# Performance work log

Measured on AMD Instinct MI355X. Metric: run time of the kernel, lower is better.

The kernel has to match this reference:

```python
import jax, jax.numpy as jnp
import numpy as np
import math

D_MODEL = 1024
NUM_HEADS = 16
D_HEAD = D_MODEL // NUM_HEADS  # 64
B, S = 2, 1024


def setup_inputs() -> dict:
    key = jax.random.key(0)
    ks = jax.random.split(key, 11)
    s = 1.0 / math.sqrt(D_MODEL)
    inp = {
        "Q": jax.random.normal(ks[0], (B, S, D_MODEL), jnp.float32),
        "K": jax.random.normal(ks[1], (B, S, D_MODEL), jnp.float32),
        "V": jax.random.normal(ks[2], (B, S, D_MODEL), jnp.float32),
        "Wq": jax.random.normal(ks[3], (D_MODEL, D_MODEL), jnp.float32) * s,
        "bq": jnp.zeros((D_MODEL,), jnp.float32),
        "Wk": jax.random.normal(ks[4], (D_MODEL, D_MODEL), jnp.float32) * s,
        "bk": jnp.zeros((D_MODEL,), jnp.float32),
        "Wv": jax.random.normal(ks[5], (D_MODEL, D_MODEL), jnp.float32) * s,
        "bv": jnp.zeros((D_MODEL,), jnp.float32),
        "Wo": jax.random.normal(ks[6], (D_MODEL, D_MODEL), jnp.float32) * s,
        "bo": jnp.zeros((D_MODEL,), jnp.float32),
    }
    return inp


def _linear(x, W, b):
    # torch nn.Linear: x @ W.T + b
    return jnp.einsum("bsd,ed->bse", x, W) + b


def _split_heads(x):
    # Faithful to original: view(b, s, d_head, num_heads).transpose(1, 2)
    # -> 'heads' axis has size d_head, per-head dim is num_heads.
    b, s, _ = x.shape
    return x.reshape(b, s, D_HEAD, NUM_HEADS).transpose(0, 2, 1, 3)  # [b, d_head, s, num_heads]


def reference(Q, K, V, Wq, bq, Wk, bk, Wv, bv, Wo, bo):
    q = _split_heads(_linear(Q, Wq, bq))  # [b, h=d_head, s, e=num_heads]
    k = _split_heads(_linear(K, Wk, bk))
    v = _split_heads(_linear(V, Wv, bv))
    scale = 1.0 / math.sqrt(D_MODEL)  # original scales by sqrt(d_model)
    scores = jnp.einsum("bhqe,bhke->bhqk", q, k) * scale
    attn = jax.nn.softmax(scores, axis=-1)
    ctx = jnp.einsum("bhqk,bhke->bhqe", attn, v)  # [b, d_head, s, num_heads]
    # combine_heads: transpose(1,2) then flatten last two dims
    b, h, s, e = ctx.shape
    merged = ctx.transpose(0, 2, 1, 3).reshape(b, s, h * e)
    return _linear(merged, Wo, bo)
```

## Files before the change

### kernel.cpp

```cpp
#include <hip/hip_runtime.h>
#include <cstdint>
#include <cstddef>
#include <math.h>

typedef _Float16 f16;
typedef _Float16 f16x8 __attribute__((ext_vector_type(8)));
typedef _Float16 f16x4 __attribute__((ext_vector_type(4)));
typedef float f32x4 __attribute__((ext_vector_type(4)));
typedef float f32x16 __attribute__((ext_vector_type(16)));

#define MFMA16(A, B, C) __builtin_amdgcn_mfma_f32_16x16x32_f16((A), (B), (C), 0, 0, 0)
#define MFMA32(A, B, C) __builtin_amdgcn_mfma_f32_32x32x16_f16((A), (B), (C), 0, 0, 0)

#if __has_builtin(__builtin_amdgcn_exp2f)
#define EXP2(x) __builtin_amdgcn_exp2f(x)
#else
#define EXP2(x) exp2f(x)
#endif

__device__ __forceinline__ f16x8 ld8(const f16* p) { return *(const f16x8*)p; }
__device__ __forceinline__ void st8(f16* p, f16x8 v) { *(f16x8*)p = v; }
__device__ __forceinline__ void st4(f16* p, f16x4 v) { *(f16x4*)p = v; }

__device__ __forceinline__ void gll16(const f16* g, f16* l) {
    __builtin_amdgcn_global_load_lds(
        (__attribute__((address_space(1))) void*)(uintptr_t)g,
        (__attribute__((address_space(3))) void*)(unsigned)(uintptr_t)l,
        16, 0, 0);
}

__global__ __launch_bounds__(256) void cast_all(
    const float* __restrict__ Q, const float* __restrict__ K, const float* __restrict__ V,
    const float* __restrict__ Wq, const float* __restrict__ Wk, const float* __restrict__ Wv,
    const float* __restrict__ Wo, f16* __restrict__ dst)
{
    size_t e = ((size_t)blockIdx.x * 256 + threadIdx.x) * 8;
    const float* s; size_t r;
    if (e < 2097152)      { s = Q;  r = e; }
    else if (e < 4194304) { s = K;  r = e - 2097152; }
    else if (e < 6291456) { s = V;  r = e - 4194304; }
    else if (e < 7340032) { s = Wq; r = e - 6291456; }
    else if (e < 8388608) { s = Wk; r = e - 7340032; }
    else if (e < 9437184) { s = Wv; r = e - 8388608; }
    else                  { s = Wo; r = e - 9437184; }
    float4 a = *(const float4*)(s + r);
    float4 b = *(const float4*)(s + r + 4);
    f16x8 o;
    o[0]=(f16)a.x; o[1]=(f16)a.y; o[2]=(f16)a.z; o[3]=(f16)a.w;
    o[4]=(f16)b.x; o[5]=(f16)b.y; o[6]=(f16)b.z; o[7]=(f16)b.w;
    st8(dst + e, o);
}

__global__ __launch_bounds__(256) void qkv_gemm(
    const f16* __restrict__ ws, const float* __restrict__ bq,
    const float* __restrict__ bk, const float* __restrict__ bv,
    f16* __restrict__ outbase)
{
    const int bx = blockIdx.x, bm = blockIdx.y;
    const int mat = bx >> 3, bn = bx & 7;
    const f16* A  = ws + (size_t)mat * 2097152;
    const f16* Bw = ws + 6291456 + (size_t)mat * 1048576;
    const float* bias = (mat == 0) ? bq : (mat == 1) ? bk : bv;
    f16* C = outbase + (size_t)mat * 2097152;

    __shared__ f16 As[2 * 4096];
    __shared__ f16 Bs[2 * 8192];
    const int t = threadIdx.x;
    const int w = t >> 6, lane = t & 63, lg = lane >> 4, ll = lane & 15;
    const int swz = ((lane & 7) ^ (lane >> 3)) * 8;

    const f16* Ap = A  + (size_t)(bm * 64  + w * 8 + (lane >> 3)) * 1024 + swz;
    const f16* Bp = Bw + (size_t)(bn * 128 + w * 8 + (lane >> 3)) * 1024 + swz;

    f32x4 acc[4][2] = {};
    const int ll7 = ll & 7;

    {
        gll16(Ap,         &As[w * 512]);
        gll16(Ap + 32768, &As[2048 + w * 512]);
        #pragma unroll
        for (int q = 0; q < 4; ++q)
            gll16(Bp + q * 32768, &Bs[q * 2048 + w * 512]);
    }

    #pragma unroll 2
    for (int kt = 0; kt < 16; ++kt) {
        const int cur = kt & 1;
        __syncthreads();
        if (kt < 15) {
            const f16* Ak = Ap + (kt + 1) * 64;
            const f16* Bk = Bp + (kt + 1) * 64;
            f16* Ad = &As[(cur ^ 1) * 4096 + w * 512];
            f16* Bd = &Bs[(cur ^ 1) * 8192 + w * 512];
            gll16(Ak,         Ad);
            gll16(Ak + 32768, Ad + 2048);
            #pragma unroll
            for (int q = 0; q < 4; ++q)
                gll16(Bk + q * 32768, Bd + q * 2048);
        }
        const f16* Ac = &As[cur * 4096];
        const f16* Bc = &Bs[cur * 8192];
        #pragma unroll
        for (int ks = 0; ks < 2; ++ks) {
            f16x8 af[4], bf[2];
            #pragma unroll
            for (int i = 0; i < 4; ++i)
                af[i] = ld8(&Ac[(i * 16 + ll) * 64 + (((ks * 4 + lg) ^ ll7) * 8)]);
            #pragma unroll
            for (int j = 0; j < 2; ++j)
                bf[j] = ld8(&Bc[(w * 32 + j * 16 + ll) * 64 + (((ks * 4 + lg) ^ ll7) * 8)]);
            #pragma unroll
            for (int i = 0; i < 4; ++i)
                #pragma unroll
                for (int j = 0; j < 2; ++j)
                    acc[i][j] = MFMA16(af[i], bf[j], acc[i][j]);
        }
    }

    const float qscale = 0.04508422002778009f;
    #pragma unroll
    for (int j = 0; j < 2; ++j) {
        const int n = bn * 128 + w * 32 + j * 16 + ll;
        const float bv_ = bias[n];
        if (mat == 0) {
            #pragma unroll
            for (int i = 0; i < 4; ++i) {
                const int m0 = bm * 64 + i * 16 + lg * 4;
                #pragma unroll
                for (int r = 0; r < 4; ++r)
                    C[(size_t)(m0 + r) * 1024 + n] = (f16)((acc[i][j][r] + bv_) * qscale);
            }
        } else if (mat == 1) {
            #pragma unroll
            for (int i = 0; i < 4; ++i) {
                const int m0 = bm * 64 + i * 16 + lg * 4;
                #pragma unroll
                for (int r = 0; r < 4; ++r)
                    C[(size_t)(m0 + r) * 1024 + n] = (f16)(acc[i][j][r] + bv_);
            }
        } else {
            #pragma unroll
            for (int i = 0; i < 4; ++i) {
                const int m0 = bm * 64 + i * 16 + lg * 4;
                const int bb = m0 >> 10, s0 = m0 & 1023;
                f16x4 pv;
                pv[0] = (f16)(acc[i][j][0] + bv_);
                pv[1] = (f16)(acc[i][j][1] + bv_);
                pv[2] = (f16)(acc[i][j][2] + bv_);
                pv[3] = (f16)(acc[i][j][3] + bv_);
                st4(C + ((size_t)((bb * 64 + (n >> 4)) * 16 + (n & 15))) * 1024 + s0, pv);
            }
        }
    }
}

__global__ __launch_bounds__(256, 4) void attn(
    const f16* __restrict__ qlin, const f16* __restrict__ klin,
    const f16* __restrict__ vT, f16* __restrict__ merged)
{
    __shared__ f16 Ks[2][2048];
    __shared__ f16 Vs[2][2176];
    __shared__ f16 Ps[4][1280];

    const int t = threadIdx.x;
    const int w = t >> 6, lane = t & 63;
    const int l5 = lane & 31, hh = lane >> 5, lg = (lane >> 4) & 3, ll = lane & 15;
    const int h = blockIdx.x, qt = blockIdx.y, b = blockIdx.z;

    const int rowQ0 = b * 1024 + qt * 128;
    const int colh = h * 16;

    f16x8 qf = ld8(qlin + (size_t)(rowQ0 + w * 32 + l5) * 1024 + colh + hh * 8);

    const int sp = ((lane & 7) - (lane >> 3)) & 7;
    const f16* kptr = klin + (size_t)(b * 1024 + w * 32 + (lane >> 3) * 4 + (sp >> 1)) * 1024
                      + colh + (sp & 1) * 8;
    const int ve = t >> 4, vk = (t & 15) * 8;
    const f16* vptr = vT + (size_t)((b * 64 + h) * 16 + ve) * 1024 + vk;
    f16* vdst0 = &Vs[0][ve * 136 + vk];
    f16* vdst1 = &Vs[1][ve * 136 + vk];

    int offKa[4];
    #pragma unroll
    for (int mt = 0; mt < 4; ++mt) {
        const int r = mt * 32 + l5, g = r >> 2;
        offKa[mt] = g * 64 + (((((r & 3) * 2 + hh) + g) & 7) * 8);
    }

    float lsum = 0.f;
    f32x4 O0 = {}, O1 = {};
    f16* Pw = Ps[w];

    f16x8 vv = ld8(vptr);
    gll16(kptr, &Ks[0][w * 512]);
    st8(vdst0, vv);

    for (int kt = 0; kt < 8; ++kt) {
        const int cur = kt & 1;
        if (kt < 7) vv = ld8(vptr + (kt + 1) * 128);
        __syncthreads();
        if (kt < 7) {
            gll16(kptr + (size_t)(kt + 1) * 131072, &Ks[cur ^ 1][w * 512]);
            st8(cur ? vdst0 : vdst1, vv);
        }

        #pragma unroll
        for (int mt = 0; mt < 4; ++mt) {
            f16x8 ka = ld8(&Ks[cur][offKa[mt]]);
            f32x16 Sz = {};
            f32x16 S = MFMA32(ka, qf, Sz);

            #pragma unroll
            for (int g = 0; g < 4; ++g) {
                float p0 = EXP2(S[4 * g + 0]);
                float p1 = EXP2(S[4 * g + 1]);
                float p2 = EXP2(S[4 * g + 2]);
                float p3 = EXP2(S[4 * g + 3]);
                lsum += (p0 + p1) + (p2 + p3);
                f16x4 pk;
                pk[0] = (f16)p0; pk[1] = (f16)p1; pk[2] = (f16)p2; pk[3] = (f16)p3;
                st4(&Pw[l5 * 40 + g * 8 + hh * 4], pk);
            }

            f16x8 va  = ld8(&Vs[cur][ll * 136 + mt * 32 + lg * 8]);
            f16x8 pb0 = ld8(&Pw[ll * 40 + lg * 8]);
            f16x8 pb1 = ld8(&Pw[(16 + ll) * 40 + lg * 8]);
            O0 = MFMA16(va, pb0, O0);
            O1 = MFMA16(va, pb1, O1);
        }
    }

    lsum += __shfl_xor(lsum, 32);
    const float i0 = 1.f / __shfl(lsum, ll);
    const float i1 = 1.f / __shfl(lsum, 16 + ll);

    f16x4 o0, o1;
    o0[0]=(f16)(O0[0]*i0); o0[1]=(f16)(O0[1]*i0); o0[2]=(f16)(O0[2]*i0); o0[3]=(f16)(O0[3]*i0);
    o1[0]=(f16)(O1[0]*i1); o1[1]=(f16)(O1[1]*i1); o1[2]=(f16)(O1[2]*i1); o1[3]=(f16)(O1[3]*i1);
    const size_t q0 = rowQ0 + w * 32 + ll;
    st4(merged + q0 * 1024 + colh + lg * 4, o0);
    st4(merged + (q0 + 16) * 1024 + colh + lg * 4, o1);
}

__global__ __launch_bounds__(256) void o_gemm(
    const f16* __restrict__ A, const f16* __restrict__ Bw,
    const float* __restrict__ bias, float* __restrict__ Cf)
{
    const int bn = blockIdx.x, bm = blockIdx.y;
    __shared__ f16 As[2 * 4096];
    __shared__ f16 Bs[2 * 4096];
    const int t = threadIdx.x;
    const int w = t >> 6, lane = t & 63, lg = lane >> 4, ll = lane & 15;
    const int swz = ((lane & 7) ^ (lane >> 3)) * 8;

    const f16* Ap = A  + (size_t)(bm * 64 + w * 8 + (lane >> 3)) * 1024 + swz;
    const f16* Bp = Bw + (size_t)(bn * 64 + w * 8 + (lane >> 3)) * 1024 + swz;

    f32x4 acc[4] = {};
    const int ll7 = ll & 7;

    {
        gll16(Ap,         &As[w * 512]);
        gll16(Ap + 32768, &As[2048 + w * 512]);
        gll16(Bp,         &Bs[w * 512]);
        gll16(Bp + 32768, &Bs[2048 + w * 512]);
    }

    #pragma unroll 2
    for (int kt = 0; kt < 16; ++kt) {
        const int cur = kt & 1;
        __syncthreads();
        if (kt < 15) {
            const f16* Ak = Ap + (kt + 1) * 64;
            const f16* Bk = Bp + (kt + 1) * 64;
            f16* Ad = &As[(cur ^ 1) * 4096 + w * 512];
            f16* Bd = &Bs[(cur ^ 1) * 4096 + w * 512];
            gll16(Ak,         Ad);
            gll16(Ak + 32768, Ad + 2048);
            gll16(Bk,         Bd);
            gll16(Bk + 32768, Bd + 2048);
        }
        const f16* Ac = &As[cur * 4096];
        const f16* Bc = &Bs[cur * 4096];
        #pragma unroll
        for (int ks = 0; ks < 2; ++ks) {
            f16x8 af[4], bf;
            #pragma unroll
            for (int i = 0; i < 4; ++i)
                af[i] = ld8(&Ac[(i * 16 + ll) * 64 + (((ks * 4 + lg) ^ ll7) * 8)]);
            bf = ld8(&Bc[(w * 16 + ll) * 64 + (((ks * 4 + lg) ^ ll7) * 8)]);
            #pragma unroll
            for (int i = 0; i < 4; ++i)
                acc[i] = MFMA16(af[i], bf, acc[i]);
        }
    }

    const int n = bn * 64 + w * 16 + ll;
    const float bv_ = bias[n];
    #pragma unroll
    for (int i = 0; i < 4; ++i) {
        const int m0 = bm * 64 + i * 16 + lg * 4;
        #pragma unroll
        for (int r = 0; r < 4; ++r)
            Cf[(size_t)(m0 + r) * 1024 + n] = acc[i][r] + bv_;
    }
}

extern "C" void kernel_launch(void* const* d_in, const int* in_sizes, int n_in,
                              void* d_out, int out_size, void* d_ws, size_t ws_size,
                              hipStream_t stream) {
    (void)in_sizes; (void)n_in; (void)out_size; (void)ws_size;
    const float* Q  = (const float*)d_in[0];
    const float* K  = (const float*)d_in[1];
    const float* V  = (const float*)d_in[2];
    const float* Wq = (const float*)d_in[3];
    const float* bq = (const float*)d_in[4];
    const float* Wk = (const float*)d_in[5];
    const float* bk = (const float*)d_in[6];
    const float* Wv = (const float*)d_in[7];
    const float* bv = (const float*)d_in[8];
    const float* Wo = (const float*)d_in[9];
    const float* bo = (const float*)d_in[10];
    float* out = (float*)d_out;

    f16* ws = (f16*)d_ws;
    f16* qlin   = ws + 10485760;
    f16* klin   = ws + 12582912;
    f16* vT     = ws + 14680064;
    f16* merged = ws + 16777216;
    f16* Woc    = ws + 9437184;

    cast_all<<<5120, 256, 0, stream>>>(Q, K, V, Wq, Wk, Wv, Wo, ws);
    qkv_gemm<<<dim3(24, 32), 256, 0, stream>>>(ws, bq, bk, bv, qlin);
    attn<<<dim3(64, 8, 2), 256, 0, stream>>>(qlin, klin, vT, merged);
    o_gemm<<<dim3(16, 32), 256, 0, stream>>>(merged, Woc, bo, out);
}
```

Measured before the change: 159.8 us.

## Fuse fp32-to-fp16 casts into GEMM tile loads and drop cast kernel

```diff
diff --git a/kernel.cpp b/kernel.cpp
--- a/kernel.cpp
+++ b/kernel.cpp
@@ -29,128 +29,120 @@
         16, 0, 0);
 }
 
-__global__ __launch_bounds__(256) void cast_all(
-    const float* __restrict__ Q, const float* __restrict__ K, const float* __restrict__ V,
-    const float* __restrict__ Wq, const float* __restrict__ Wk, const float* __restrict__ Wv,
-    const float* __restrict__ Wo, f16* __restrict__ dst)
-{
-    size_t e = ((size_t)blockIdx.x * 256 + threadIdx.x) * 8;
-    const float* s; size_t r;
-    if (e < 2097152)      { s = Q;  r = e; }
-    else if (e < 4194304) { s = K;  r = e - 2097152; }
-    else if (e < 6291456) { s = V;  r = e - 4194304; }
-    else if (e < 7340032) { s = Wq; r = e - 6291456; }
-    else if (e < 8388608) { s = Wk; r = e - 7340032; }
-    else if (e < 9437184) { s = Wv; r = e - 8388608; }
-    else                  { s = Wo; r = e - 9437184; }
-    float4 a = *(const float4*)(s + r);
-    float4 b = *(const float4*)(s + r + 4);
+__device__ __forceinline__ f16x8 cvt8(float4 a, float4 b) {
     f16x8 o;
     o[0]=(f16)a.x; o[1]=(f16)a.y; o[2]=(f16)a.z; o[3]=(f16)a.w;
     o[4]=(f16)b.x; o[5]=(f16)b.y; o[6]=(f16)b.z; o[7]=(f16)b.w;
-    st8(dst + e, o);
-}
-
-__global__ __launch_bounds__(256) void qkv_gemm(
-    const f16* __restrict__ ws, const float* __restrict__ bq,
-    const float* __restrict__ bk, const float* __restrict__ bv,
+    return o;
+}
+
+#define QSCALE 0.04508422002778009f
+
+__global__ __launch_bounds__(256, 3) void qkv_gemm(
+    const float* __restrict__ Qf, const float* __restrict__ Kf, const float* __restrict__ Vf,
+    const float* __restrict__ Wq, const float* __restrict__ Wk, const float* __restrict__ Wv,
+    const float* __restrict__ bq, const float* __restrict__ bk, const float* __restrict__ bv,
     f16* __restrict__ outbase)
 {
     const int bx = blockIdx.x, bm = blockIdx.y;
     const int mat = bx >> 3, bn = bx & 7;
-    const f16* A  = ws + (size_t)mat * 2097152;
-    const f16* Bw = ws + 6291456 + (size_t)mat * 1048576;
+    const float* A = (mat == 0) ? Qf : (mat == 1) ? Kf : Vf;
+    const float* W = (mat == 0) ? Wq : (mat == 1) ? Wk : Wv;
     const float* bias = (mat == 0) ? bq : (mat == 1) ? bk : bv;
     f16* C = outbase + (size_t)mat * 2097152;
 
-    __shared__ f16 As[2 * 4096];
-    __shared__ f16 Bs[2 * 8192];
+    __shared__ f16 As[2][64 * 68];
+    __shared__ f16 Bs[2][128 * 68];
+
     const int t = threadIdx.x;
-    const int w = t >> 6, lane = t & 63, lg = lane >> 4, ll = lane & 15;
-    const int swz = ((lane & 7) ^ (lane >> 3)) * 8;
-
-    const f16* Ap = A  + (size_t)(bm * 64  + w * 8 + (lane >> 3)) * 1024 + swz;
-    const f16* Bp = Bw + (size_t)(bn * 128 + w * 8 + (lane >> 3)) * 1024 + swz;
-
-    f32x4 acc[4][2] = {};
-    const int ll7 = ll & 7;
-
-    {
-        gll16(Ap,         &As[w * 512]);
-        gll16(Ap + 32768, &As[2048 + w * 512]);
-        #pragma unroll
-        for (int q = 0; q < 4; ++q)
-            gll16(Bp + q * 32768, &Bs[q * 2048 + w * 512]);
-    }
-
-    #pragma unroll 2
+    const int w = t >> 6, lane = t & 63, l5 = lane & 31, hh = lane >> 5;
+
+    const int ra = t >> 2, qa = t & 3;
+    const int rb = t >> 1, hb = t & 1;
+    const float* Ag = A + (size_t)(bm * 64 + ra) * 1024 + qa * 16;
+    const float* Bg = W + (size_t)(bn * 128 + rb) * 1024 + hb * 32;
+    const int aoff = ra * 68 + qa * 16;
+    const int boff = rb * 68 + hb * 32;
+
+    f32x16 acc[2] = {};
+    float4 pa[4], pb[8];
+
+    #pragma unroll
+    for (int i = 0; i < 4; ++i) pa[i] = *(const float4*)(Ag + i * 4);
+    #pragma unroll
+    for (int i = 0; i < 8; ++i) pb[i] = *(const float4*)(Bg + i * 4);
+    st8(&As[0][aoff],     cvt8(pa[0], pa[1]));
+    st8(&As[0][aoff + 8], cvt8(pa[2], pa[3]));
+    st8(&Bs[0][boff],      cvt8(pb[0], pb[1]));
+    st8(&Bs[0][boff + 8],  cvt8(pb[2], pb[3]));
+    st8(&Bs[0][boff + 16], cvt8(pb[4], pb[5]));
+    st8(&Bs[0][boff + 24], cvt8(pb[6], pb[7]));
+    __syncthreads();
+
     for (int kt = 0; kt < 16; ++kt) {
         const int cur = kt & 1;
+        if (kt < 15) {
+            const float* Ak = Ag + (kt + 1) * 64;
+            const float* Bk = Bg + (kt + 1) * 64;
+            #pragma unroll
+            for (int i = 0; i < 4; ++i) pa[i] = *(const float4*)(Ak + i * 4);
+            #pragma unroll
+            for (int i = 0; i < 8; ++i) pb[i] = *(const float4*)(Bk + i * 4);
+        }
+        #pragma unroll
+        for (int ks = 0; ks < 4; ++ks) {
+            f16x8 bfr = ld8(&Bs[cur][(w * 32 + l5) * 68 + ks * 16 + hh * 8]);
+            f16x8 af0 = ld8(&As[cur][ l5        * 68 + ks * 16 + hh * 8]);
+            f16x8 af1 = ld8(&As[cur][(32 + l5)  * 68 + ks * 16 + hh * 8]);
+            acc[0] = MFMA32(af0, bfr, acc[0]);
+            acc[1] = MFMA32(af1, bfr, acc[1]);
+        }
+        if (kt < 15) {
+            f16* Ad = &As[cur ^ 1][aoff];
+            f16* Bd = &Bs[cur ^ 1][boff];
+            st8(Ad,     cvt8(pa[0], pa[1]));
+            st8(Ad + 8, cvt8(pa[2], pa[3]));
+            st8(Bd,      cvt8(pb[0], pb[1]));
+            st8(Bd + 8,  cvt8(pb[2], pb[3]));
+            st8(Bd + 16, cvt8(pb[4], pb[5]));
+            st8(Bd + 24, cvt8(pb[6], pb[7]));
+        }
         __syncthreads();
-        if (kt < 15) {
-            const f16* Ak = Ap + (kt + 1) * 64;
-            const f16* Bk = Bp + (kt + 1) * 64;
-            f16* Ad = &As[(cur ^ 1) * 4096 + w * 512];
-            f16* Bd = &Bs[(cur ^ 1) * 8192 + w * 512];
-            gll16(Ak,         Ad);
-            gll16(Ak + 32768, Ad + 2048);
-            #pragma unroll
-            for (int q = 0; q < 4; ++q)
-                gll16(Bk + q * 32768, Bd + q * 2048);
-        }
-        const f16* Ac = &As[cur * 4096];
-        const f16* Bc = &Bs[cur * 8192];
-        #pragma unroll
-        for (int ks = 0; ks < 2; ++ks) {
-            f16x8 af[4], bf[2];
-            #pragma unroll
-            for (int i = 0; i < 4; ++i)
-                af[i] = ld8(&Ac[(i * 16 + ll) * 64 + (((ks * 4 + lg) ^ ll7) * 8)]);
-            #pragma unroll
-            for (int j = 0; j < 2; ++j)
-                bf[j] = ld8(&Bc[(w * 32 + j * 16 + ll) * 64 + (((ks * 4 + lg) ^ ll7) * 8)]);
-            #pragma unroll
-            for (int i = 0; i < 4; ++i)
-                #pragma unroll
-                for (int j = 0; j < 2; ++j)
-                    acc[i][j] = MFMA16(af[i], bf[j], acc[i][j]);
-        }
-    }
-
-    const float qscale = 0.04508422002778009f;
-    #pragma unroll
-    for (int j = 0; j < 2; ++j) {
-        const int n = bn * 128 + w * 32 + j * 16 + ll;
-        const float bv_ = bias[n];
-        if (mat == 0) {
-            #pragma unroll
-            for (int i = 0; i < 4; ++i) {
-                const int m0 = bm * 64 + i * 16 + lg * 4;
-                #pragma unroll
-                for (int r = 0; r < 4; ++r)
-                    C[(size_t)(m0 + r) * 1024 + n] = (f16)((acc[i][j][r] + bv_) * qscale);
+    }
+
+    const int n = bn * 128 + w * 32 + l5;
+    const float bv_ = bias[n];
+    if (mat == 0) {
+        #pragma unroll
+        for (int i = 0; i < 2; ++i)
+            #pragma unroll
+            for (int r = 0; r < 16; ++r) {
+                const int m = bm * 64 + i * 32 + (r & 3) + 8 * (r >> 2) + 4 * hh;
+                C[(size_t)m * 1024 + n] = (f16)((acc[i][r] + bv_) * QSCALE);
             }
-        } else if (mat == 1) {
-            #pragma unroll
-            for (int i = 0; i < 4; ++i) {
-                const int m0 = bm * 64 + i * 16 + lg * 4;
-                #pragma unroll
-                for (int r = 0; r < 4; ++r)
-                    C[(size_t)(m0 + r) * 1024 + n] = (f16)(acc[i][j][r] + bv_);
+    } else if (mat == 1) {
+        #pragma unroll
+        for (int i = 0; i < 2; ++i)
+            #pragma unroll
+            for (int r = 0; r < 16; ++r) {
+                const int m = bm * 64 + i * 32 + (r & 3) + 8 * (r >> 2) + 4 * hh;
+                C[(size_t)m * 1024 + n] = (f16)(acc[i][r] + bv_);
             }
-        } else {
-            #pragma unroll
-            for (int i = 0; i < 4; ++i) {
-                const int m0 = bm * 64 + i * 16 + lg * 4;
+    } else {
+        const int hN = n >> 4, eN = n & 15;
+        #pragma unroll
+        for (int i = 0; i < 2; ++i)
+            #pragma unroll
+            for (int g = 0; g < 4; ++g) {
+                const int m0 = bm * 64 + i * 32 + 8 * g + 4 * hh;
                 const int bb = m0 >> 10, s0 = m0 & 1023;
                 f16x4 pv;
-                pv[0] = (f16)(acc[i][j][0] + bv_);
-                pv[1] = (f16)(acc[i][j][1] + bv_);
-                pv[2] = (f16)(acc[i][j][2] + bv_);
-                pv[3] = (f16)(acc[i][j][3] + bv_);
-                st4(C + ((size_t)((bb * 64 + (n >> 4)) * 16 + (n & 15))) * 1024 + s0, pv);
+                pv[0] = (f16)(acc[i][4 * g + 0] + bv_);
+                pv[1] = (f16)(acc[i][4 * g + 1] + bv_);
+                pv[2] = (f16)(acc[i][4 * g + 2] + bv_);
+                pv[3] = (f16)(acc[i][4 * g + 3] + bv_);
+                st4(C + ((size_t)((bb * 64 + hN) * 16 + eN)) * 1024 + s0, pv);
             }
-        }
     }
 }
 
@@ -243,66 +235,61 @@
 }
 
 __global__ __launch_bounds__(256) void o_gemm(
-    const f16* __restrict__ A, const f16* __restrict__ Bw,
-    const float* __restrict__ bias, float* __restrict__ Cf)
+    const f16* __restrict__ Am, const float* __restrict__ Wo,
+    const float* __restrict__ bo, float* __restrict__ Cf)
 {
     const int bn = blockIdx.x, bm = blockIdx.y;
-    __shared__ f16 As[2 * 4096];
-    __shared__ f16 Bs[2 * 4096];
+    __shared__ f16 As[2][64 * 68];
+    __shared__ f16 Bs[2][64 * 68];
     const int t = threadIdx.x;
-    const int w = t >> 6, lane = t & 63, lg = lane >> 4, ll = lane & 15;
-    const int swz = ((lane & 7) ^ (lane >> 3)) * 8;
-
-    const f16* Ap = A  + (size_t)(bm * 64 + w * 8 + (lane >> 3)) * 1024 + swz;
-    const f16* Bp = Bw + (size_t)(bn * 64 + w * 8 + (lane >> 3)) * 1024 + swz;
-
-    f32x4 acc[4] = {};
-    const int ll7 = ll & 7;
-
-    {
-        gll16(Ap,         &As[w * 512]);
-        gll16(Ap + 32768, &As[2048 + w * 512]);
-        gll16(Bp,         &Bs[w * 512]);
-        gll16(Bp + 32768, &Bs[2048 + w * 512]);
-    }
-
-    #pragma unroll 2
+    const int w = t >> 6, lane = t & 63, l5 = lane & 31, hh = lane >> 5;
+    const int wr = w >> 1, wc = w & 1;
+
+    const int ra = t >> 2, qa = t & 3;
+    const f16*   Ag = Am + (size_t)(bm * 64 + ra) * 1024 + qa * 16;
+    const float* Bg = Wo + (size_t)(bn * 64 + ra) * 1024 + qa * 16;
+    const int soff = ra * 68 + qa * 16;
+
+    f32x16 acc = {};
+    f16x8 la0, la1;
+    float4 pb[4];
+
+    la0 = ld8(Ag); la1 = ld8(Ag + 8);
+    #pragma unroll
+    for (int i = 0; i < 4; ++i) pb[i] = *(const float4*)(Bg + i * 4);
+    st8(&As[0][soff], la0); st8(&As[0][soff + 8], la1);
+    st8(&Bs[0][soff],     cvt8(pb[0], pb[1]));
+    st8(&Bs[0][soff + 8], cvt8(pb[2], pb[3]));
+    __syncthreads();
+
     for (int kt = 0; kt < 16; ++kt) {
         const int cur = kt & 1;
+        if (kt < 15) {
+            la0 = ld8(Ag + (kt + 1) * 64);
+            la1 = ld8(Ag + (kt + 1) * 64 + 8);
+            #pragma unroll
+            for (int i = 0; i < 4; ++i) pb[i] = *(const float4*)(Bg + (kt + 1) * 64 + i * 4);
+        }
+        #pragma unroll
+        for (int ks = 0; ks < 4; ++ks) {
+            f16x8 af = ld8(&As[cur][(wr * 32 + l5) * 68 + ks * 16 + hh * 8]);
+            f16x8 bf = ld8(&Bs[cur][(wc * 32 + l5) * 68 + ks * 16 + hh * 8]);
+            acc = MFMA32(af, bf, acc);
+        }
+        if (kt < 15) {
+            st8(&As[cur ^ 1][soff], la0); st8(&As[cur ^ 1][soff + 8], la1);
+            st8(&Bs[cur ^ 1][soff],     cvt8(pb[0], pb[1]));
+            st8(&Bs[cur ^ 1][soff + 8], cvt8(pb[2], pb[3]));
+        }
         __syncthreads();
-        if (kt < 15) {
-            const f16* Ak = Ap + (kt + 1) * 64;
-            const f16* Bk = Bp + (kt + 1) * 64;
-            f16* Ad = &As[(cur ^ 1) * 4096 + w * 512];
-            f16* Bd = &Bs[(cur ^ 1) * 4096 + w * 512];
-            gll16(Ak,         Ad);
-            gll16(Ak + 32768, Ad + 2048);
-            gll16(Bk,         Bd);
-            gll16(Bk + 32768, Bd + 2048);
-        }
-        const f16* Ac = &As[cur * 4096];
-        const f16* Bc = &Bs[cur * 4096];
-        #pragma unroll
-        for (int ks = 0; ks < 2; ++ks) {
-            f16x8 af[4], bf;
-            #pragma unroll
-            for (int i = 0; i < 4; ++i)
-                af[i] = ld8(&Ac[(i * 16 + ll) * 64 + (((ks * 4 + lg) ^ ll7) * 8)]);
-            bf = ld8(&Bc[(w * 16 + ll) * 64 + (((ks * 4 + lg) ^ ll7) * 8)]);
-            #pragma unroll
-            for (int i = 0; i < 4; ++i)
-                acc[i] = MFMA16(af[i], bf, acc[i]);
-        }
-    }
-
-    const int n = bn * 64 + w * 16 + ll;
-    const float bv_ = bias[n];
-    #pragma unroll
-    for (int i = 0; i < 4; ++i) {
-        const int m0 = bm * 64 + i * 16 + lg * 4;
-        #pragma unroll
-        for (int r = 0; r < 4; ++r)
-            Cf[(size_t)(m0 + r) * 1024 + n] = acc[i][r] + bv_;
+    }
+
+    const int n = bn * 64 + wc * 32 + l5;
+    const float bv_ = bo[n];
+    #pragma unroll
+    for (int r = 0; r < 16; ++r) {
+        const int m = bm * 64 + wr * 32 + (r & 3) + 8 * (r >> 2) + 4 * hh;
+        Cf[(size_t)m * 1024 + n] = acc[r] + bv_;
     }
 }
 
@@ -324,14 +311,12 @@
     float* out = (float*)d_out;
 
     f16* ws = (f16*)d_ws;
-    f16* qlin   = ws + 10485760;
-    f16* klin   = ws + 12582912;
-    f16* vT     = ws + 14680064;
-    f16* merged = ws + 16777216;
-    f16* Woc    = ws + 9437184;
-
-    cast_all<<<5120, 256, 0, stream>>>(Q, K, V, Wq, Wk, Wv, Wo, ws);
-    qkv_gemm<<<dim3(24, 32), 256, 0, stream>>>(ws, bq, bk, bv, qlin);
+    f16* qlin   = ws;
+    f16* klin   = ws + 2097152;
+    f16* vT     = ws + 4194304;
+    f16* merged = ws + 6291456;
+
+    qkv_gemm<<<dim3(24, 32), 256, 0, stream>>>(Q, K, V, Wq, Wk, Wv, bq, bk, bv, qlin);
     attn<<<dim3(64, 8, 2), 256, 0, stream>>>(qlin, klin, vT, merged);
-    o_gemm<<<dim3(16, 32), 256, 0, stream>>>(merged, Woc, bo, out);
-}
+    o_gemm<<<dim3(16, 32), 256, 0, stream>>>(merged, Wo, bo, out);
+}
```

Result: slower. 259.7 us (+62.5%).

## Fuse cast, QKV GEMM, attention and output GEMM into one persistent kernel

Applied to the files above, without the earlier changes.

```diff
diff --git a/kernel.cpp b/kernel.cpp
--- a/kernel.cpp
+++ b/kernel.cpp
@@ -17,6 +17,8 @@
 #else
 #define EXP2(x) exp2f(x)
 #endif
+
+#define NBLK 768
 
 __device__ __forceinline__ f16x8 ld8(const f16* p) { return *(const f16x8*)p; }
 __device__ __forceinline__ void st8(f16* p, f16x8 v) { *(f16x8*)p = v; }
@@ -29,280 +31,320 @@
         16, 0, 0);
 }
 
-__global__ __launch_bounds__(256) void cast_all(
+__device__ __forceinline__ void gridbarrier(int* flags, int phase) {
+    __syncthreads();
+    if (threadIdx.x == 0) {
+        __threadfence();
+        __hip_atomic_store(&flags[blockIdx.x], phase, __ATOMIC_RELEASE,
+                           __HIP_MEMORY_SCOPE_AGENT);
+    }
+    if (threadIdx.x < 64) {
+        for (;;) {
+            int ok = 1;
+            #pragma unroll
+            for (int i = 0; i < NBLK / 64; ++i) {
+                int v = __hip_atomic_load(&flags[threadIdx.x + i * 64],
+                                          __ATOMIC_RELAXED, __HIP_MEMORY_SCOPE_AGENT);
+                ok &= (v >= phase);
+            }
+            if (__all(ok)) break;
+            __builtin_amdgcn_s_sleep(4);
+        }
+    }
+    __syncthreads();
+    __threadfence();
+}
+
+#define QSCALE 0.04508422002778009f
+
+__global__ __launch_bounds__(256, 3) void fused(
     const float* __restrict__ Q, const float* __restrict__ K, const float* __restrict__ V,
-    const float* __restrict__ Wq, const float* __restrict__ Wk, const float* __restrict__ Wv,
-    const float* __restrict__ Wo, f16* __restrict__ dst)
+    const float* __restrict__ Wq, const float* __restrict__ bq,
+    const float* __restrict__ Wk, const float* __restrict__ bk,
+    const float* __restrict__ Wv, const float* __restrict__ bv,
+    const float* __restrict__ Wo, const float* __restrict__ bo,
+    f16* __restrict__ ws, float* __restrict__ out)
 {
-    size_t e = ((size_t)blockIdx.x * 256 + threadIdx.x) * 8;
-    const float* s; size_t r;
-    if (e < 2097152)      { s = Q;  r = e; }
-    else if (e < 4194304) { s = K;  r = e - 2097152; }
-    else if (e < 6291456) { s = V;  r = e - 4194304; }
-    else if (e < 7340032) { s = Wq; r = e - 6291456; }
-    else if (e < 8388608) { s = Wk; r = e - 7340032; }
-    else if (e < 9437184) { s = Wv; r = e - 8388608; }
-    else                  { s = Wo; r = e - 9437184; }
-    float4 a = *(const float4*)(s + r);
-    float4 b = *(const float4*)(s + r + 4);
-    f16x8 o;
-    o[0]=(f16)a.x; o[1]=(f16)a.y; o[2]=(f16)a.z; o[3]=(f16)a.w;
-    o[4]=(f16)b.x; o[5]=(f16)b.y; o[6]=(f16)b.z; o[7]=(f16)b.w;
-    st8(dst + e, o);
-}
-
-__global__ __launch_bounds__(256) void qkv_gemm(
-    const f16* __restrict__ ws, const float* __restrict__ bq,
-    const float* __restrict__ bk, const float* __restrict__ bv,
-    f16* __restrict__ outbase)
-{
-    const int bx = blockIdx.x, bm = blockIdx.y;
-    const int mat = bx >> 3, bn = bx & 7;
-    const f16* A  = ws + (size_t)mat * 2097152;
-    const f16* Bw = ws + 6291456 + (size_t)mat * 1048576;
-    const float* bias = (mat == 0) ? bq : (mat == 1) ? bk : bv;
-    f16* C = outbase + (size_t)mat * 2097152;
-
-    __shared__ f16 As[2 * 4096];
-    __shared__ f16 Bs[2 * 8192];
+    __shared__ union {
+        struct { f16 As[2 * 4096]; f16 Bs[2 * 8192]; } g;
+        struct { f16 Ks[2][2048]; f16 Vs[2][2176]; f16 Ps[4][1280]; } a;
+        struct { f16 As[2 * 4096]; f16 Bs[2 * 4096]; } o;
+    } sm;
+
+    int* flags = (int*)(ws + 18874368);
     const int t = threadIdx.x;
     const int w = t >> 6, lane = t & 63, lg = lane >> 4, ll = lane & 15;
-    const int swz = ((lane & 7) ^ (lane >> 3)) * 8;
-
-    const f16* Ap = A  + (size_t)(bm * 64  + w * 8 + (lane >> 3)) * 1024 + swz;
-    const f16* Bp = Bw + (size_t)(bn * 128 + w * 8 + (lane >> 3)) * 1024 + swz;
-
-    f32x4 acc[4][2] = {};
-    const int ll7 = ll & 7;
+
+    if (t == 0)
+        __hip_atomic_store(&flags[blockIdx.x], 0, __ATOMIC_RELAXED,
+                           __HIP_MEMORY_SCOPE_AGENT);
 
     {
+        f16* dst = ws;
+        #pragma unroll
+        for (int sweep = 0; sweep < 7; ++sweep) {
+            size_t e = ((size_t)sweep * NBLK * 256 + (size_t)blockIdx.x * 256 + t) * 8;
+            if (e < 10485760) {
+                const float* s; size_t r;
+                if (e < 2097152)      { s = Q;  r = e; }
+                else if (e < 4194304) { s = K;  r = e - 2097152; }
+                else if (e < 6291456) { s = V;  r = e - 4194304; }
+                else if (e < 7340032) { s = Wq; r = e - 6291456; }
+                else if (e < 8388608) { s = Wk; r = e - 7340032; }
+                else if (e < 9437184) { s = Wv; r = e - 8388608; }
+                else                  { s = Wo; r = e - 9437184; }
+                float4 a = *(const float4*)(s + r);
+                float4 b = *(const float4*)(s + r + 4);
+                f16x8 o;
+                o[0]=(f16)a.x; o[1]=(f16)a.y; o[2]=(f16)a.z; o[3]=(f16)a.w;
+                o[4]=(f16)b.x; o[5]=(f16)b.y; o[6]=(f16)b.z; o[7]=(f16)b.w;
+                st8(dst + e, o);
+            }
+        }
+    }
+    gridbarrier(flags, 1);
+
+    {
+        const int v = blockIdx.x;
+        const int bx = v % 24, bm = v / 24;
+        const int mat = bx >> 3, bn = bx & 7;
+        const f16* A  = ws + (size_t)mat * 2097152;
+        const f16* Bw = ws + 6291456 + (size_t)mat * 1048576;
+        const float* bias = (mat == 0) ? bq : (mat == 1) ? bk : bv;
+        f16* C = ws + 10485760 + (size_t)mat * 2097152;
+
+        f16* As = sm.g.As;
+        f16* Bs = sm.g.Bs;
+        const int swz = ((lane & 7) ^ (lane >> 3)) * 8;
+
+        const f16* Ap = A  + (size_t)(bm * 64  + w * 8 + (lane >> 3)) * 1024 + swz;
+        const f16* Bp = Bw + (size_t)(bn * 128 + w * 8 + (lane >> 3)) * 1024 + swz;
+
+        f32x4 acc[4][2] = {};
+        const int ll7 = ll & 7;
+
         gll16(Ap,         &As[w * 512]);
         gll16(Ap + 32768, &As[2048 + w * 512]);
         #pragma unroll
         for (int q = 0; q < 4; ++q)
             gll16(Bp + q * 32768, &Bs[q * 2048 + w * 512]);
-    }
-
-    #pragma unroll 2
-    for (int kt = 0; kt < 16; ++kt) {
-        const int cur = kt & 1;
-        __syncthreads();
-        if (kt < 15) {
-            const f16* Ak = Ap + (kt + 1) * 64;
-            const f16* Bk = Bp + (kt + 1) * 64;
-            f16* Ad = &As[(cur ^ 1) * 4096 + w * 512];
-            f16* Bd = &Bs[(cur ^ 1) * 8192 + w * 512];
-            gll16(Ak,         Ad);
-            gll16(Ak + 32768, Ad + 2048);
+
+        #pragma unroll 2
+        for (int kt = 0; kt < 16; ++kt) {
+            const int cur = kt & 1;
+            __syncthreads();
+            if (kt < 15) {
+                const f16* Ak = Ap + (kt + 1) * 64;
+                const f16* Bk = Bp + (kt + 1) * 64;
+                f16* Ad = &As[(cur ^ 1) * 4096 + w * 512];
+                f16* Bd = &Bs[(cur ^ 1) * 8192 + w * 512];
+                gll16(Ak,         Ad);
+                gll16(Ak + 32768, Ad + 2048);
+                #pragma unroll
+                for (int q = 0; q < 4; ++q)
+                    gll16(Bk + q * 32768, Bd + q * 2048);
+            }
+            const f16* Ac = &As[cur * 4096];
+            const f16* Bc = &Bs[cur * 8192];
             #pragma unroll
-            for (int q = 0; q < 4; ++q)
-                gll16(Bk + q * 32768, Bd + q * 2048);
-        }
-        const f16* Ac = &As[cur * 4096];
-        const f16* Bc = &Bs[cur * 8192];
-        #pragma unroll
-        for (int ks = 0; ks < 2; ++ks) {
-            f16x8 af[4], bf[2];
-            #pragma unroll
-            for (int i = 0; i < 4; ++i)
-                af[i] = ld8(&Ac[(i * 16 + ll) * 64 + (((ks * 4 + lg) ^ ll7) * 8)]);
-            #pragma unroll
-            for (int j = 0; j < 2; ++j)
-                bf[j] = ld8(&Bc[(w * 32 + j * 16 + ll) * 64 + (((ks * 4 + lg) ^ ll7) * 8)]);
-            #pragma unroll
-            for (int i = 0; i < 4; ++i)
+            for (int ks = 0; ks < 2; ++ks) {
+                f16x8 af[4], bf[2];
+                #pragma unroll
+                for (int i = 0; i < 4; ++i)
+                    af[i] = ld8(&Ac[(i * 16 + ll) * 64 + (((ks * 4 + lg) ^ ll7) * 8)]);
                 #pragma unroll
                 for (int j = 0; j < 2; ++j)
-                    acc[i][j] = MFMA16(af[i], bf[j], acc[i][j]);
-        }
-    }
-
-    const float qscale = 0.04508422002778009f;
-    #pragma unroll
-    for (int j = 0; j < 2; ++j) {
-        const int n = bn * 128 + w * 32 + j * 16 + ll;
-        const float bv_ = bias[n];
-        if (mat == 0) {
-            #pragma unroll
-            for (int i = 0; i < 4; ++i) {
-                const int m0 = bm * 64 + i * 16 + lg * 4;
-                #pragma unroll
-                for (int r = 0; r < 4; ++r)
-                    C[(size_t)(m0 + r) * 1024 + n] = (f16)((acc[i][j][r] + bv_) * qscale);
-            }
-        } else if (mat == 1) {
-            #pragma unroll
-            for (int i = 0; i < 4; ++i) {
-                const int m0 = bm * 64 + i * 16 + lg * 4;
-                #pragma unroll
-                for (int r = 0; r < 4; ++r)
-                    C[(size_t)(m0 + r) * 1024 + n] = (f16)(acc[i][j][r] + bv_);
-            }
-        } else {
-            #pragma unroll
-            for (int i = 0; i < 4; ++i) {
-                const int m0 = bm * 64 + i * 16 + lg * 4;
-                const int bb = m0 >> 10, s0 = m0 & 1023;
-                f16x4 pv;
-                pv[0] = (f16)(acc[i][j][0] + bv_);
-                pv[1] = (f16)(acc[i][j][1] + bv_);
-                pv[2] = (f16)(acc[i][j][2] + bv_);
-                pv[3] = (f16)(acc[i][j][3] + bv_);
-                st4(C + ((size_t)((bb * 64 + (n >> 4)) * 16 + (n & 15))) * 1024 + s0, pv);
-            }
-        }
-    }
-}
-
-__global__ __launch_bounds__(256, 4) void attn(
-    const f16* __restrict__ qlin, const f16* __restrict__ klin,
-    const f16* __restrict__ vT, f16* __restrict__ merged)
-{
-    __shared__ f16 Ks[2][2048];
-    __shared__ f16 Vs[2][2176];
-    __shared__ f16 Ps[4][1280];
-
-    const int t = threadIdx.x;
-    const int w = t >> 6, lane = t & 63;
-    const int l5 = lane & 31, hh = lane >> 5, lg = (lane >> 4) & 3, ll = lane & 15;
-    const int h = blockIdx.x, qt = blockIdx.y, b = blockIdx.z;
-
-    const int rowQ0 = b * 1024 + qt * 128;
-    const int colh = h * 16;
-
-    f16x8 qf = ld8(qlin + (size_t)(rowQ0 + w * 32 + l5) * 1024 + colh + hh * 8);
-
-    const int sp = ((lane & 7) - (lane >> 3)) & 7;
-    const f16* kptr = klin + (size_t)(b * 1024 + w * 32 + (lane >> 3) * 4 + (sp >> 1)) * 1024
-                      + colh + (sp & 1) * 8;
-    const int ve = t >> 4, vk = (t & 15) * 8;
-    const f16* vptr = vT + (size_t)((b * 64 + h) * 16 + ve) * 1024 + vk;
-    f16* vdst0 = &Vs[0][ve * 136 + vk];
-    f16* vdst1 = &Vs[1][ve * 136 + vk];
-
-    int offKa[4];
-    #pragma unroll
-    for (int mt = 0; mt < 4; ++mt) {
-        const int r = mt * 32 + l5, g = r >> 2;
-        offKa[mt] = g * 64 + (((((r & 3) * 2 + hh) + g) & 7) * 8);
-    }
-
-    float lsum = 0.f;
-    f32x4 O0 = {}, O1 = {};
-    f16* Pw = Ps[w];
-
-    f16x8 vv = ld8(vptr);
-    gll16(kptr, &Ks[0][w * 512]);
-    st8(vdst0, vv);
-
-    for (int kt = 0; kt < 8; ++kt) {
-        const int cur = kt & 1;
-        if (kt < 7) vv = ld8(vptr + (kt + 1) * 128);
-        __syncthreads();
-        if (kt < 7) {
-            gll16(kptr + (size_t)(kt + 1) * 131072, &Ks[cur ^ 1][w * 512]);
-            st8(cur ? vdst0 : vdst1, vv);
-        }
-
+                    bf[j] = ld8(&Bc[(w * 32 + j * 16 + ll) * 64 + (((ks * 4 + lg) ^ ll7) * 8)]);
+                #pragma unroll
+                for (int i = 0; i < 4; ++i)
+                    #pragma unroll
+                    for (int j = 0; j < 2; ++j)
+                        acc[i][j] = MFMA16(af[i], bf[j], acc[i][j]);
+            }
+        }
+
+        #pragma unroll
+        for (int j = 0; j < 2; ++j) {
+            const int n = bn * 128 + w * 32 + j * 16 + ll;
+            const float bv_ = bias[n];
+            if (mat == 0) {
+                #pragma unroll
+                for (int i = 0; i < 4; ++i) {
+                    const int m0 = bm * 64 + i * 16 + lg * 4;
+                    #pragma unroll
+                    for (int r = 0; r < 4; ++r)
+                        C[(size_t)(m0 + r) * 1024 + n] = (f16)((acc[i][j][r] + bv_) * QSCALE);
+                }
+            } else if (mat == 1) {
+                #pragma unroll
+                for (int i = 0; i < 4; ++i) {
+                    const int m0 = bm * 64 + i * 16 + lg * 4;
+                    #pragma unroll
+                    for (int r = 0; r < 4; ++r)
+                        C[(size_t)(m0 + r) * 1024 + n] = (f16)(acc[i][j][r] + bv_);
+                }
+            } else {
+                #pragma unroll
+                for (int i = 0; i < 4; ++i) {
+                    const int m0 = bm * 64 + i * 16 + lg * 4;
+                    const int bb = m0 >> 10, s0 = m0 & 1023;
+                    f16x4 pv;
+                    pv[0] = (f16)(acc[i][j][0] + bv_);
+                    pv[1] = (f16)(acc[i][j][1] + bv_);
+                    pv[2] = (f16)(acc[i][j][2] + bv_);
+                    pv[3] = (f16)(acc[i][j][3] + bv_);
+                    st4(C + ((size_t)((bb * 64 + (n >> 4)) * 16 + (n & 15))) * 1024 + s0, pv);
+                }
+            }
+        }
+    }
+    gridbarrier(flags, 2);
+
+    {
+        const f16* qlin = ws + 10485760;
+        const f16* klin = ws + 12582912;
+        const f16* vT   = ws + 14680064;
+        f16* merged     = ws + 16777216;
+
+        const int l5 = lane & 31, hh = lane >> 5;
+        int offKa[4];
         #pragma unroll
         for (int mt = 0; mt < 4; ++mt) {
-            f16x8 ka = ld8(&Ks[cur][offKa[mt]]);
-            f32x16 Sz = {};
-            f32x16 S = MFMA32(ka, qf, Sz);
-
-            #pragma unroll
-            for (int g = 0; g < 4; ++g) {
-                float p0 = EXP2(S[4 * g + 0]);
-                float p1 = EXP2(S[4 * g + 1]);
-                float p2 = EXP2(S[4 * g + 2]);
-                float p3 = EXP2(S[4 * g + 3]);
-                lsum += (p0 + p1) + (p2 + p3);
-                f16x4 pk;
-                pk[0] = (f16)p0; pk[1] = (f16)p1; pk[2] = (f16)p2; pk[3] = (f16)p3;
-                st4(&Pw[l5 * 40 + g * 8 + hh * 4], pk);
-            }
-
-            f16x8 va  = ld8(&Vs[cur][ll * 136 + mt * 32 + lg * 8]);
-            f16x8 pb0 = ld8(&Pw[ll * 40 + lg * 8]);
-            f16x8 pb1 = ld8(&Pw[(16 + ll) * 40 + lg * 8]);
-            O0 = MFMA16(va, pb0, O0);
-            O1 = MFMA16(va, pb1, O1);
-        }
-    }
-
-    lsum += __shfl_xor(lsum, 32);
-    const float i0 = 1.f / __shfl(lsum, ll);
-    const float i1 = 1.f / __shfl(lsum, 16 + ll);
-
-    f16x4 o0, o1;
-    o0[0]=(f16)(O0[0]*i0); o0[1]=(f16)(O0[1]*i0); o0[2]=(f16)(O0[2]*i0); o0[3]=(f16)(O0[3]*i0);
-    o1[0]=(f16)(O1[0]*i1); o1[1]=(f16)(O1[1]*i1); o1[2]=(f16)(O1[2]*i1); o1[3]=(f16)(O1[3]*i1);
-    const size_t q0 = rowQ0 + w * 32 + ll;
-    st4(merged + q0 * 1024 + colh + lg * 4, o0);
-    st4(merged + (q0 + 16) * 1024 + colh + lg * 4, o1);
-}
-
-__global__ __launch_bounds__(256) void o_gemm(
-    const f16* __restrict__ A, const f16* __restrict__ Bw,
-    const float* __restrict__ bias, float* __restrict__ Cf)
-{
-    const int bn = blockIdx.x, bm = blockIdx.y;
-    __shared__ f16 As[2 * 4096];
-    __shared__ f16 Bs[2 * 4096];
-    const int t = threadIdx.x;
-    const int w = t >> 6, lane = t & 63, lg = lane >> 4, ll = lane & 15;
-    const int swz = ((lane & 7) ^ (lane >> 3)) * 8;
-
-    const f16* Ap = A  + (size_t)(bm * 64 + w * 8 + (lane >> 3)) * 1024 + swz;
-    const f16* Bp = Bw + (size_t)(bn * 64 + w * 8 + (lane >> 3)) * 1024 + swz;
-
-    f32x4 acc[4] = {};
-    const int ll7 = ll & 7;
-
-    {
+            const int r = mt * 32 + l5, g = r >> 2;
+            offKa[mt] = g * 64 + (((((r & 3) * 2 + hh) + g) & 7) * 8);
+        }
+        const int sp = ((lane & 7) - (lane >> 3)) & 7;
+
+        for (int v = blockIdx.x; v < 1024; v += NBLK) {
+            __syncthreads();
+            const int h = v & 63, qt = (v >> 6) & 7, b = v >> 9;
+            const int rowQ0 = b * 1024 + qt * 128;
+            const int colh = h * 16;
+
+            f16x8 qf = ld8(qlin + (size_t)(rowQ0 + w * 32 + l5) * 1024 + colh + hh * 8);
+
+            const f16* kptr = klin + (size_t)(b * 1024 + w * 32 + (lane >> 3) * 4 + (sp >> 1)) * 1024
+                              + colh + (sp & 1) * 8;
+            const int ve = t >> 4, vk = (t & 15) * 8;
+            const f16* vptr = vT + (size_t)((b * 64 + h) * 16 + ve) * 1024 + vk;
+            f16* vdst0 = &sm.a.Vs[0][ve * 136 + vk];
+            f16* vdst1 = &sm.a.Vs[1][ve * 136 + vk];
+
+            float lsum = 0.f;
+            f32x4 O0 = {}, O1 = {};
+            f16* Pw = sm.a.Ps[w];
+
+            f16x8 vv = ld8(vptr);
+            gll16(kptr, &sm.a.Ks[0][w * 512]);
+            st8(vdst0, vv);
+
+            for (int kt = 0; kt < 8; ++kt) {
+                const int cur = kt & 1;
+                if (kt < 7) vv = ld8(vptr + (kt + 1) * 128);
+                __syncthreads();
+                if (kt < 7) {
+                    gll16(kptr + (size_t)(kt + 1) * 131072, &sm.a.Ks[cur ^ 1][w * 512]);
+                    st8(cur ? vdst0 : vdst1, vv);
+                }
+
+                #pragma unroll
+                for (int mt = 0; mt < 4; ++mt) {
+                    f16x8 ka = ld8(&sm.a.Ks[cur][offKa[mt]]);
+                    f32x16 Sz = {};
+                    f32x16 S = MFMA32(ka, qf, Sz);
+
+                    #pragma unroll
+                    for (int g = 0; g < 4; ++g) {
+                        float p0 = EXP2(S[4 * g + 0]);
+                        float p1 = EXP2(S[4 * g + 1]);
+                        float p2 = EXP2(S[4 * g + 2]);
+                        float p3 = EXP2(S[4 * g + 3]);
+                        lsum += (p0 + p1) + (p2 + p3);
+                        f16x4 pk;
+                        pk[0] = (f16)p0; pk[1] = (f16)p1; pk[2] = (f16)p2; pk[3] = (f16)p3;
+                        st4(&Pw[l5 * 40 + g * 8 + hh * 4], pk);
+                    }
+
+                    f16x8 va  = ld8(&sm.a.Vs[cur][ll * 136 + mt * 32 + lg * 8]);
+                    f16x8 pb0 = ld8(&Pw[ll * 40 + lg * 8]);
+                    f16x8 pb1 = ld8(&Pw[(16 + ll) * 40 + lg * 8]);
+                    O0 = MFMA16(va, pb0, O0);
+                    O1 = MFMA16(va, pb1, O1);
+                }
+            }
+
+            lsum += __shfl_xor(lsum, 32);
+            const float i0 = 1.f / __shfl(lsum, ll);
+            const float i1 = 1.f / __shfl(lsum, 16 + ll);
+
+            f16x4 o0, o1;
+            o0[0]=(f16)(O0[0]*i0); o0[1]=(f16)(O0[1]*i0); o0[2]=(f16)(O0[2]*i0); o0[3]=(f16)(O0[3]*i0);
+            o1[0]=(f16)(O1[0]*i1); o1[1]=(f16)(O1[1]*i1); o1[2]=(f16)(O1[2]*i1); o1[3]=(f16)(O1[3]*i1);
+            const size_t q0 = rowQ0 + w * 32 + ll;
+            st4(merged + q0 * 1024 + colh + lg * 4, o0);
+            st4(merged + (q0 + 16) * 1024 + colh + lg * 4, o1);
+        }
+    }
+    gridbarrier(flags, 3);
+
+    if (blockIdx.x < 512) {
+        const f16* Am  = ws + 16777216;
+        const f16* Bw  = ws + 9437184;
+        const int bn = blockIdx.x & 15, bm = blockIdx.x >> 4;
+
+        f16* As = sm.o.As;
+        f16* Bs = sm.o.Bs;
+        const int swz = ((lane & 7) ^ (lane >> 3)) * 8;
+
+        const f16* Ap = Am + (size_t)(bm * 64 + w * 8 + (lane >> 3)) * 1024 + swz;
+        const f16* Bp = Bw + (size_t)(bn * 64 + w * 8 + (lane >> 3)) * 1024 + swz;
+
+        f32x4 acc[4] = {};
+        const int ll7 = ll & 7;
+
         gll16(Ap,         &As[w * 512]);
         gll16(Ap + 32768, &As[2048 + w * 512]);
         gll16(Bp,         &Bs[w * 512]);
         gll16(Bp + 32768, &Bs[2048 + w * 512]);
-    }
-
-    #pragma unroll 2
-    for (int kt = 0; kt < 16; ++kt) {
-        const int cur = kt & 1;
-        __syncthreads();
-        if (kt < 15) {
-            const f16* Ak = Ap + (kt + 1) * 64;
-            const f16* Bk = Bp + (kt + 1) * 64;
-            f16* Ad = &As[(cur ^ 1) * 4096 + w * 512];
-            f16* Bd = &Bs[(cur ^ 1) * 4096 + w * 512];
-            gll16(Ak,         Ad);
-            gll16(Ak + 32768, Ad + 2048);
-            gll16(Bk,         Bd);
-            gll16(Bk + 32768, Bd + 2048);
-        }
-        const f16* Ac = &As[cur * 4096];
-        const f16* Bc = &Bs[cur * 4096];
-        #pragma unroll
-        for (int ks = 0; ks < 2; ++ks) {
-            f16x8 af[4], bf;
+
+        #pragma unroll 2
+        for (int kt = 0; kt < 16; ++kt) {
+            const int cur = kt & 1;
+            __syncthreads();
+            if (kt < 15) {
+                const f16* Ak = Ap + (kt + 1) * 64;
+                const f16* Bk = Bp + (kt + 1) * 64;
+                f16* Ad = &As[(cur ^ 1) * 4096 + w * 512];
+                f16* Bd = &Bs[(cur ^ 1) * 4096 + w * 512];
+                gll16(Ak,         Ad);
+                gll16(Ak + 32768, Ad + 2048);
+                gll16(Bk,         Bd);
+                gll16(Bk + 32768, Bd + 2048);
+            }
+            const f16* Ac = &As[cur * 4096];
+            const f16* Bc = &Bs[cur * 4096];
             #pragma unroll
-            for (int i = 0; i < 4; ++i)
-                af[i] = ld8(&Ac[(i * 16 + ll) * 64 + (((ks * 4 + lg) ^ ll7) * 8)]);
-            bf = ld8(&Bc[(w * 16 + ll) * 64 + (((ks * 4 + lg) ^ ll7) * 8)]);
+            for (int ks = 0; ks < 2; ++ks) {
+                f16x8 af[4], bf;
+                #pragma unroll
+                for (int i = 0; i < 4; ++i)
+                    af[i] = ld8(&Ac[(i * 16 + ll) * 64 + (((ks * 4 + lg) ^ ll7) * 8)]);
+                bf = ld8(&Bc[(w * 16 + ll) * 64 + (((ks * 4 + lg) ^ ll7) * 8)]);
+                #pragma unroll
+                for (int i = 0; i < 4; ++i)
+                    acc[i] = MFMA16(af[i], bf, acc[i]);
+            }
+        }
+
+        const int n = bn * 64 + w * 16 + ll;
+        const float bv_ = bo[n];
+        #pragma unroll
+        for (int i = 0; i < 4; ++i) {
+            const int m0 = bm * 64 + i * 16 + lg * 4;
             #pragma unroll
-            for (int i = 0; i < 4; ++i)
-                acc[i] = MFMA16(af[i], bf, acc[i]);
-        }
-    }
-
-    const int n = bn * 64 + w * 16 + ll;
-    const float bv_ = bias[n];
-    #pragma unroll
-    for (int i = 0; i < 4; ++i) {
-        const int m0 = bm * 64 + i * 16 + lg * 4;
-        #pragma unroll
-        for (int r = 0; r < 4; ++r)
-            Cf[(size_t)(m0 + r) * 1024 + n] = acc[i][r] + bv_;
+            for (int r = 0; r < 4; ++r)
+                out[(size_t)(m0 + r) * 1024 + n] = acc[i][r] + bv_;
+        }
     }
 }
 
@@ -322,16 +364,7 @@
     const float* Wo = (const float*)d_in[9];
     const float* bo = (const float*)d_in[10];
     float* out = (float*)d_out;
-
     f16* ws = (f16*)d_ws;
-    f16* qlin   = ws + 10485760;
-    f16* klin   = ws + 12582912;
-    f16* vT     = ws + 14680064;
-    f16* merged = ws + 16777216;
-    f16* Woc    = ws + 9437184;
-
-    cast_all<<<5120, 256, 0, stream>>>(Q, K, V, Wq, Wk, Wv, Wo, ws);
-    qkv_gemm<<<dim3(24, 32), 256, 0, stream>>>(ws, bq, bk, bv, qlin);
-    attn<<<dim3(64, 8, 2), 256, 0, stream>>>(qlin, klin, vT, merged);
-    o_gemm<<<dim3(16, 32), 256, 0, stream>>>(merged, Woc, bo, out);
+
+    fused<<<NBLK, 256, 0, stream>>>(Q, K, V, Wq, bq, Wk, bk, Wv, bv, Wo, bo, ws, out);
 }
```

New measurement: 423.0 us. 165% more time.
